# Performance work log

Hardware: AMD Instinct MI355X
Metric: run time of the kernel (lower is better)

Reference implementation:

```python
import jax, jax.numpy as jnp
import numpy as np
import math

C = 512         # embed_size
L_V = 196       # num_patches (square -> no cls token)
B_V = 64        # image batch
B_T = 32        # caption batch
N_WORD = 24     # words per caption (all cap_lens equal)
SPARSE_RATIO = 0.5
AGGR_RATIO = 0.5
NUM_KEEP = math.ceil(L_V * SPARSE_RATIO)            # 98 kept tokens
KEEPED = int(L_V * AGGR_RATIO * SPARSE_RATIO)       # 49 aggregated tokens
HIDDEN = int(C * 0.2)                               # 102 MLP hidden (dim_ratio=0.2)
LAMBDA = 4.0                                        # xattn softmax temperature
LN_EPS = 1e-5


def l2norm(x, axis=-1):
    n = jnp.linalg.norm(x, axis=axis, keepdims=True)
    return x / jnp.maximum(n, 1e-12)


def setup_inputs() -> dict:
    key = jax.random.key(0)
    ks = jax.random.split(key, 4)
    img_embs = jax.random.normal(ks[0], (B_V, L_V, C), dtype=jnp.float32)
    cap_embs = jax.random.normal(ks[1], (B_T, N_WORD, C), dtype=jnp.float32)
    cap_lens = jnp.full((B_T,), N_WORD, dtype=jnp.int64 if jax.config.read('jax_enable_x64') else jnp.int32)
    # TokenAggregation params: LayerNorm -> Linear(C,HIDDEN) -> GELU -> Linear(HIDDEN,KEEPED), scale
    ln_gamma = jnp.ones((C,), jnp.float32)
    ln_beta = jnp.zeros((C,), jnp.float32)
    W1 = jax.random.normal(ks[2], (C, HIDDEN), dtype=jnp.float32) * 0.02
    b1 = jnp.zeros((HIDDEN,), jnp.float32)
    W2 = jax.random.normal(ks[3], (HIDDEN, KEEPED), dtype=jnp.float32) * 0.02
    b2 = jnp.zeros((KEEPED,), jnp.float32)
    scale = jnp.ones((), jnp.float32)
    return dict(img_embs=img_embs, cap_embs=cap_embs, cap_lens=cap_lens,
                ln_gamma=ln_gamma, ln_beta=ln_beta, W1=W1, b1=b1, W2=W2, b2=b2, scale=scale)


def _forward(img_embs, cap_embs, ln_gamma, ln_beta, W1, b1, W2, b2, scale):
    # --- global attention scores (computed under no_grad in torch) ---
    img_norm = l2norm(img_embs)                                   # (Bv,Lv,C)
    cap_norm = l2norm(cap_embs)                                   # (Bt,W,C)
    img_glo = l2norm(jnp.mean(img_embs, axis=1, keepdims=True))   # (Bv,1,C)
    self_attn = jnp.sum(img_glo * img_norm, axis=-1)              # (Bv,Lv)
    cap_glo = l2norm(jnp.mean(cap_embs, axis=1))                  # (Bt,C)
    cross_attn = jnp.einsum('tc,vlc->tvl', cap_glo, img_norm)     # (Bt,Bv,Lv)
    score = jax.lax.stop_gradient(self_attn[None] + cross_attn)   # (Bt,Bv,Lv)

    # --- TokenSparse: sort, split keep / non-keep ---
    order = jnp.argsort(-score, axis=-1)                          # descending indices
    score_sort = jnp.take_along_axis(score, order, axis=-1)
    keep_idx = order[..., :NUM_KEEP]                              # (Bt,Bv,K)
    non_idx = order[..., NUM_KEEP:]                               # (Bt,Bv,Lv-K)
    rank = jnp.argsort(order, axis=-1)                            # inverse permutation
    score_mask = (rank < NUM_KEEP).astype(score.dtype)            # (Bt,Bv,Lv)

    bidx = jnp.arange(B_V)[None, :, None]
    select_tokens = img_embs[bidx, keep_idx]                      # (Bt,Bv,K,C) gather
    non_tokens = img_embs[bidx, non_idx]                          # (Bt,Bv,Lv-K,C)
    non_w = jax.nn.softmax(score_sort[..., NUM_KEEP:], axis=-1)   # (Bt,Bv,Lv-K)
    extra_token = jnp.sum(non_tokens * non_w[..., None], axis=-2, keepdims=True)  # (Bt,Bv,1,C)

    # --- TokenAggregation: LN -> MLP -> softmax -> bmm ---
    mu = jnp.mean(select_tokens, axis=-1, keepdims=True)
    var = jnp.var(select_tokens, axis=-1, keepdims=True)
    xn = (select_tokens - mu) * jax.lax.rsqrt(var + LN_EPS) * ln_gamma + ln_beta
    h = jax.nn.gelu(jnp.einsum('tvkc,ch->tvkh', xn, W1) + b1, approximate=False)
    w = jnp.einsum('tvkh,hp->tvkp', h, W2) + b2                   # (Bt,Bv,K,P)
    w = jnp.swapaxes(w, -1, -2) * scale                           # (Bt,Bv,P,K)
    w = jax.nn.softmax(w, axis=-1)
    aggr = jnp.einsum('tvpk,tvkc->tvpc', w, select_tokens)        # (Bt,Bv,P,C)

    keep_tokens = jnp.concatenate([aggr, extra_token], axis=2)    # (Bt,Bv,P+1,C)
    sel_norm = l2norm(keep_tokens)

    # --- mask_xattn_one_text: SCAN-style t2i attention ---
    sims = jnp.einsum('twc,tvpc->tvwp', cap_norm, sel_norm)       # (Bt,Bv,W,P+1)
    attn = jax.nn.softmax(LAMBDA * sims, axis=-1)
    ctx = l2norm(jnp.einsum('tvwp,tvpc->tvwc', attn, sel_norm))   # (Bt,Bv,W,C)
    word_sim = jnp.einsum('twc,tvwc->tvw', cap_norm, ctx)         # (Bt,Bv,W)
    sim = jnp.mean(word_sim, axis=-1)                             # (Bt,Bv)
    improve_sims = sim.T                                          # (Bv,Bt)
    return improve_sims, score_mask


def reference(img_embs, cap_embs, cap_lens, ln_gamma, ln_beta, W1, b1, W2, b2, scale):
    # cap_lens are all N_WORD (constant), so the per-caption loop is fully vectorized.
    return _forward(img_embs, cap_embs, ln_gamma, ln_beta, W1, b1, W2, b2, scale)
```

## Files before the change

### kernel.cpp

```cpp
#include <hip/hip_runtime.h>
#include <hip/hip_bf16.h>
#include <math.h>

#define CDIM 512
#define LV 196
#define BV 64
#define BT 32
#define NW 24
#define NKEEP 98
#define NNON 98
#define KEEPED 49
#define HID 102
#define LAMBDA_ 4.0f
#define LN_EPS_ 1e-5f

#define WS_CAPNORM 0
#define WS_CAPGLO  (WS_CAPNORM + BT*NW*CDIM)
#define WS_IMGGLO  (WS_CAPGLO + BT*CDIM)
#define WS_INVN    (WS_IMGGLO + BV*CDIM)
#define WS_WLOG    (WS_INVN + BV*LV)
#define WS_SCORE   (WS_WLOG + BV*LV*KEEPED)
#define WS_END     (WS_SCORE + BT*BV*LV)
#define WS_IMGT_B  ((size_t)WS_END * 4)
#define TOKPAD 224
#define WS_NEED_B  (WS_IMGT_B + (size_t)BV * CDIM * TOKPAD * 2)
#define WS_W1T_B   ((size_t)WS_SCORE * 4)
#define WS_W2T_B   (WS_W1T_B + (size_t)112 * 512 * 2)
#define WS_IPART   WS_WLOG

typedef short v8s __attribute__((ext_vector_type(8)));
typedef float v4f __attribute__((ext_vector_type(4)));
#define MFMA16(a, b, c) __builtin_amdgcn_mfma_f32_16x16x32_bf16((a), (b), (c), 0, 0, 0)

#define WA_STR 232
#define TOK_STR 40
#define SEL_STR 520
#define G_STR 66
#define XN_STR 520
#define HB_STR 136

#define SELQ_STR 136
#define CAPQ_STR 136
#define K4_SMEM   51968
#define OFF_SEL   0
#define OFF_WA    19216
#define OFF_CAPQ  19216
#define OFF_SIMS  19216
#define OFF_G     27408
#define OFF_SC    48912
#define OFF_KIDX  49696
#define OFF_NIDX  50088
#define OFF_CNT   50480
#define OFF_WK    50496
#define OFF_RED   50896
#define OFF_POOL2 51408
#define OFF_INV   51664

__device__ __forceinline__ ushort bfb(float f) {
  __hip_bfloat16 h = __float2bfloat16(f);
  union { __hip_bfloat16 h; ushort u; } cv; cv.h = h; return cv.u;
}

__global__ __launch_bounds__(512) void k0_prep(const float* __restrict__ img,
                                               const float* __restrict__ W1,
                                               const float* __restrict__ W2,
                                               float* __restrict__ ws) {
  int v = blockIdx.x, kt = blockIdx.y, c = threadIdx.x;
  if (kt == 7) {
    if (v < 56) {
      #pragma unroll
      for (int r = 0; r < 2; ++r) {
        int h = v * 2 + r;
        float val = (h < HID) ? W1[(size_t)c * HID + h] : 0.f;
        ((ushort*)((char*)ws + WS_W1T_B))[(size_t)h * 512 + c] = bfb(val);
      }
    } else {
      for (int e = c; e < 1024; e += 512) {
        int idx = (v - 56) * 1024 + e;
        int p = idx >> 7, h = idx & 127;
        float val = (p < KEEPED && h < HID) ? W2[(size_t)h * KEEPED + p] : 0.f;
        ((ushort*)((char*)ws + WS_W2T_B))[(size_t)p * 128 + h] = bfb(val);
      }
    }
    return;
  }
  float x[32];
  #pragma unroll
  for (int kk = 0; kk < 32; ++kk) {
    int tok = kt * 32 + kk;
    x[kk] = (tok < LV) ? img[((size_t)v * LV + tok) * CDIM + c] : 0.f;
  }
  {
    float s = 0.f;
    #pragma unroll
    for (int kk = 0; kk < 32; ++kk) s += x[kk];
    ws[WS_IPART + ((size_t)kt * BV + v) * CDIM + c] = s;
  }
  __hip_bfloat16* imgT = (__hip_bfloat16*)((char*)ws + WS_IMGT_B);
  uint* dst = (uint*)(imgT + ((size_t)v * CDIM + c) * TOKPAD + kt * 32);
  #pragma unroll
  for (int g = 0; g < 4; ++g) {
    uint4 u;
    u.x = (uint)bfb(x[g*8+0]) | ((uint)bfb(x[g*8+1]) << 16);
    u.y = (uint)bfb(x[g*8+2]) | ((uint)bfb(x[g*8+3]) << 16);
    u.z = (uint)bfb(x[g*8+4]) | ((uint)bfb(x[g*8+5]) << 16);
    u.w = (uint)bfb(x[g*8+6]) | ((uint)bfb(x[g*8+7]) << 16);
    *(uint4*)(dst + g * 4) = u;
  }
}

__global__ __launch_bounds__(512) void k5_prep(const float* __restrict__ W1,
                                               const float* __restrict__ W2,
                                               float* __restrict__ ws) {
  int b = blockIdx.x, tid = threadIdx.x;
  if (b < 112) {
    int h = b;
    float val = (h < HID) ? W1[(size_t)tid * HID + h] : 0.f;
    ((ushort*)((char*)ws + WS_W1T_B))[(size_t)h * 512 + tid] = bfb(val);
  } else {
    int p = b - 112;
    if (tid < 128) {
      int h = tid;
      float val = (p < KEEPED && h < HID) ? W2[(size_t)h * KEEPED + p] : 0.f;
      ((ushort*)((char*)ws + WS_W2T_B))[(size_t)p * 128 + h] = bfb(val);
    }
  }
}

template<int BIG>
__global__ __launch_bounds__(256) void k1_glo(const float* __restrict__ img,
                                              const float* __restrict__ cap,
                                              float* __restrict__ ws) {
  __shared__ float red[256];
  __shared__ float s_part[4 * CDIM];
  __shared__ float s_glo[CDIM];
  int b = blockIdx.x, tid = threadIdx.x;
  if (b < BT) {
    int t = b;
    int wv = tid >> 6, lane = tid & 63;
    int cb = lane * 8;
    float4 sA = make_float4(0.f,0.f,0.f,0.f), sB = make_float4(0.f,0.f,0.f,0.f);
    for (int w = wv; w < NW; w += 4) {
      const float* p = cap + ((size_t)t * NW + w) * CDIM + cb;
      float4 xa = *(const float4*)p;
      float4 xb = *(const float4*)(p + 4);
      float ss = xa.x*xa.x + xa.y*xa.y + xa.z*xa.z + xa.w*xa.w
               + xb.x*xb.x + xb.y*xb.y + xb.z*xb.z + xb.w*xb.w;
      #pragma unroll
      for (int off = 32; off > 0; off >>= 1) ss += __shfl_xor(ss, off, 64);
      float inv = 1.f / fmaxf(sqrtf(ss), 1e-12f);
      float* q = ws + WS_CAPNORM + ((size_t)t * NW + w) * CDIM + cb;
      *(float4*)q       = make_float4(xa.x*inv, xa.y*inv, xa.z*inv, xa.w*inv);
      *(float4*)(q + 4) = make_float4(xb.x*inv, xb.y*inv, xb.z*inv, xb.w*inv);
      sA.x += xa.x; sA.y += xa.y; sA.z += xa.z; sA.w += xa.w;
      sB.x += xb.x; sB.y += xb.y; sB.z += xb.z; sB.w += xb.w;
    }
    *(float4*)&s_part[wv * CDIM + cb]     = sA;
    *(float4*)&s_part[wv * CDIM + cb + 4] = sB;
    __syncthreads();
    if (tid < 128) {
      float4 g = make_float4(0.f, 0.f, 0.f, 0.f);
      #pragma unroll
      for (int w2 = 0; w2 < 4; ++w2) {
        float4 pv = *(const float4*)&s_part[w2 * CDIM + tid * 4];
        g.x += pv.x; g.y += pv.y; g.z += pv.z; g.w += pv.w;
      }
      g.x /= (float)NW; g.y /= (float)NW; g.z /= (float)NW; g.w /= (float)NW;
      *(float4*)&s_glo[tid * 4] = g;
      red[tid] = g.x*g.x + g.y*g.y + g.z*g.z + g.w*g.w;
    }
    __syncthreads();
    for (int off = 64; off > 0; off >>= 1) {
      if (tid < off) red[tid] += red[tid + off];
      __syncthreads();
    }
    float inv = 1.f / fmaxf(sqrtf(red[0]), 1e-12f);
    if (tid < 128) {
      float4 g = *(const float4*)&s_glo[tid * 4];
      *(float4*)(ws + WS_CAPGLO + (size_t)t * CDIM + tid * 4) =
          make_float4(g.x*inv, g.y*inv, g.z*inv, g.w*inv);
    }
  } else if (BIG) {
    int v = b - BT;
    int c0 = tid, c1 = tid + 256;
    float s0 = 0.f, s1 = 0.f;
    #pragma unroll
    for (int kt = 0; kt < 7; ++kt) {
      s0 += ws[WS_IPART + ((size_t)kt * BV + v) * CDIM + c0];
      s1 += ws[WS_IPART + ((size_t)kt * BV + v) * CDIM + c1];
    }
    float g0 = s0 / (float)LV, g1 = s1 / (float)LV;
    red[tid] = g0 * g0 + g1 * g1;
    __syncthreads();
    for (int off = 128; off > 0; off >>= 1) {
      if (tid < off) red[tid] += red[tid + off];
      __syncthreads();
    }
    float inv = 1.f / fmaxf(sqrtf(red[0]), 1e-12f);
    float* q = ws + WS_IMGGLO + (size_t)v * CDIM;
    q[c0] = g0 * inv; q[c1] = g1 * inv;
  } else {
    int v = b - BT;
    int wv = tid >> 6, lane = tid & 63;
    int cb = lane * 8;
    const float* base = img + (size_t)v * LV * CDIM;
    float4 sA = make_float4(0.f,0.f,0.f,0.f), sB = make_float4(0.f,0.f,0.f,0.f);
    int l0 = wv * 49;
    for (int l = l0; l < l0 + 49; ++l) {
      const float* p = base + (size_t)l * CDIM + cb;
      float4 xa = *(const float4*)p;
      float4 xb = *(const float4*)(p + 4);
      sA.x += xa.x; sA.y += xa.y; sA.z += xa.z; sA.w += xa.w;
      sB.x += xb.x; sB.y += xb.y; sB.z += xb.z; sB.w += xb.w;
    }
    *(float4*)&s_part[wv * CDIM + cb]     = sA;
    *(float4*)&s_part[wv * CDIM + cb + 4] = sB;
    __syncthreads();
    if (tid < 128) {
      float4 g = make_float4(0.f, 0.f, 0.f, 0.f);
      #pragma unroll
      for (int w2 = 0; w2 < 4; ++w2) {
        float4 pv = *(const float4*)&s_part[w2 * CDIM + tid * 4];
        g.x += pv.x; g.y += pv.y; g.z += pv.z; g.w += pv.w;
      }
      g.x /= (float)LV; g.y /= (float)LV; g.z /= (float)LV; g.w /= (float)LV;
      *(float4*)&s_glo[tid * 4] = g;
      red[tid] = g.x*g.x + g.y*g.y + g.z*g.z + g.w*g.w;
    }
    __syncthreads();
    for (int off = 64; off > 0; off >>= 1) {
      if (tid < off) red[tid] += red[tid + off];
      __syncthreads();
    }
    float inv = 1.f / fmaxf(sqrtf(red[0]), 1e-12f);
    if (tid < 128) {
      float4 g = *(const float4*)&s_glo[tid * 4];
      *(float4*)(ws + WS_IMGGLO + (size_t)v * CDIM + tid * 4) =
          make_float4(g.x*inv, g.y*inv, g.z*inv, g.w*inv);
    }
  }
}

__global__ __launch_bounds__(512, 4) void k2_mlp(const float* __restrict__ img,
                                                 const float* __restrict__ gamma,
                                                 const float* __restrict__ beta,
                                                 const float* __restrict__ b1,
                                                 const float* __restrict__ b2,
                                                 float* __restrict__ ws) {
  __shared__ __align__(16) __hip_bfloat16 s_xn[32 * XN_STR];
  __hip_bfloat16* s_hb = s_xn;

  int v = blockIdx.x, seg = blockIdx.y;
  int l0 = seg * 28;
  int tid = threadIdx.x, wv = tid >> 6, lane = tid & 63;
  int quad = lane >> 4, l15 = lane & 15, koff = quad * 8;
  const __hip_bfloat16* W1T = (const __hip_bfloat16*)((const char*)ws + WS_W1T_B);
  const __hip_bfloat16* W2T = (const __hip_bfloat16*)((const char*)ws + WS_W2T_B);

  int cb = lane * 8;
  float4 g4a = *(const float4*)(gamma + cb);
  float4 g4b = *(const float4*)(gamma + cb + 4);
  float4 b4a = *(const float4*)(beta + cb);
  float4 b4b = *(const float4*)(beta + cb + 4);
  for (int tok = wv; tok < 28; tok += 8) {
    const float* p = img + ((size_t)v * LV + l0 + tok) * CDIM + cb;
    float4 xa = *(const float4*)p;
    float4 xb = *(const float4*)(p + 4);
    float s  = xa.x + xa.y + xa.z + xa.w + xb.x + xb.y + xb.z + xb.w;
    float sq = xa.x*xa.x + xa.y*xa.y + xa.z*xa.z + xa.w*xa.w
             + xb.x*xb.x + xb.y*xb.y + xb.z*xb.z + xb.w*xb.w;
    #pragma unroll
    for (int off = 32; off > 0; off >>= 1) { s += __shfl_xor(s, off, 64); sq += __shfl_xor(sq, off, 64); }
    float mean = s / (float)CDIM;
    float var = sq / (float)CDIM - mean * mean;
    float rstd = 1.f / sqrtf(var + LN_EPS_);
    if (lane == 0) ws[WS_INVN + (size_t)v * LV + l0 + tok] = 1.f / fmaxf(sqrtf(sq), 1e-12f);
    float f[8];
    f[0] = (xa.x - mean) * rstd * g4a.x + b4a.x;
    f[1] = (xa.y - mean) * rstd * g4a.y + b4a.y;
    f[2] = (xa.z - mean) * rstd * g4a.z + b4a.z;
    f[3] = (xa.w - mean) * rstd * g4a.w + b4a.w;
    f[4] = (xb.x - mean) * rstd * g4b.x + b4b.x;
    f[5] = (xb.y - mean) * rstd * g4b.y + b4b.y;
    f[6] = (xb.z - mean) * rstd * g4b.z + b4b.z;
    f[7] = (xb.w - mean) * rstd * g4b.w + b4b.w;
    uint4 u;
    u.x = (uint)bfb(f[0]) | ((uint)bfb(f[1]) << 16);
    u.y = (uint)bfb(f[2]) | ((uint)bfb(f[3]) << 16);
    u.z = (uint)bfb(f[4]) | ((uint)bfb(f[5]) << 16);
    u.w = (uint)bfb(f[6]) | ((uint)bfb(f[7]) << 16);
    *(uint4*)(s_xn + (size_t)tok * XN_STR + cb) = u;
  }
  __syncthreads();

  v4f c1[2];
  int mt_[2], nt_[2];
  #pragma unroll
  for (int i = 0; i < 2; ++i) {
    int idx = wv + 8 * i; if (idx > 13) idx = 13;
    mt_[i] = idx / 7; nt_[i] = idx % 7;
    c1[i] = (v4f){0.f, 0.f, 0.f, 0.f};
  }
  for (int ks = 0; ks < 16; ++ks) {
    #pragma unroll
    for (int i = 0; i < 2; ++i) {
      v8s a  = *(const v8s*)(s_xn + (size_t)(mt_[i] * 16 + l15) * XN_STR + ks * 32 + koff);
      v8s bb = *(const v8s*)(W1T + (size_t)(nt_[i] * 16 + l15) * 512 + ks * 32 + koff);
      c1[i] = MFMA16(a, bb, c1[i]);
    }
  }
  __syncthreads();

  #pragma unroll
  for (int i = 0; i < 2; ++i) {
    int idx = wv + 8 * i;
    if (idx < 14) {
      int h = nt_[i] * 16 + l15;
      float bias = (h < HID) ? b1[h] : 0.f;
      #pragma unroll
      for (int reg = 0; reg < 4; ++reg) {
        int row = mt_[i] * 16 + quad * 4 + reg;
        float x = c1[i][reg] + bias;
        float gl = (h < HID) ? 0.5f * x * (1.f + erff(x * 0.70710678118654752f)) : 0.f;
        s_hb[(size_t)row * HB_STR + h] = __float2bfloat16(gl);
      }
    }
  }
  for (int i = tid; i < 32 * 16; i += 512)
    s_hb[(size_t)(i >> 4) * HB_STR + 112 + (i & 15)] = __float2bfloat16(0.f);
  __syncthreads();

  int m2 = wv >> 2, n2 = wv & 3;
  v4f c2 = (v4f){0.f, 0.f, 0.f, 0.f};
  for (int ks = 0; ks < 4; ++ks) {
    v8s a  = *(const v8s*)(s_hb + (size_t)(m2 * 16 + l15) * HB_STR + ks * 32 + koff);
    v8s bb = *(const v8s*)(W2T + (size_t)(n2 * 16 + l15) * 128 + ks * 32 + koff);
    c2 = MFMA16(a, bb, c2);
  }
  {
    int p = n2 * 16 + l15;
    if (p < KEEPED) {
      float bias = b2[p];
      #pragma unroll
      for (int reg = 0; reg < 4; ++reg) {
        int tok = m2 * 16 + quad * 4 + reg;
        if (tok < 28)
          ws[WS_WLOG + ((size_t)v * LV + l0 + tok) * KEEPED + p] = c2[reg] + bias;
      }
    }
  }
}

__global__ __launch_bounds__(512) void k3_score(const float* __restrict__ img,
                                                float* __restrict__ ws) {
  __shared__ __align__(16) float qt[33 * 64];
  __shared__ __align__(16) float xt[64 * 66];
  __shared__ float dself[64];
  int v = blockIdx.x;
  int t0 = blockIdx.y * 64;
  int tid = threadIdx.x;
  int tloc = tid & 63, qg = tid >> 6;
  float acc[5];
  #pragma unroll
  for (int i = 0; i < 5; ++i) acc[i] = 0.f;
  const float* capglo = ws + WS_CAPGLO;
  const float* imgglo = ws + WS_IMGGLO + (size_t)v * CDIM;

  for (int ct = 0; ct < 8; ++ct) {
    for (int i = tid; i < 33 * 64; i += 512) {
      int q = i >> 6, cc = i & 63;
      qt[i] = (q < 32) ? capglo[(size_t)q * CDIM + ct * 64 + cc] : imgglo[ct * 64 + cc];
    }
    for (int i = tid; i < 64 * 64; i += 512) {
      int tok = i >> 6, cc = i & 63;
      int l = t0 + tok;
      xt[tok * 66 + cc] = (l < LV) ? img[((size_t)v * LV + l) * CDIM + ct * 64 + cc] : 0.f;
    }
    __syncthreads();
    for (int cc2 = 0; cc2 < 32; ++cc2) {
      float2 xv = *(const float2*)&xt[tloc * 66 + cc2 * 2];
      #pragma unroll
      for (int qi = 0; qi < 5; ++qi) {
        int q = qg + 8 * qi;
        if (q < 33) {
          float2 qv = *(const float2*)&qt[q * 64 + cc2 * 2];
          acc[qi] += qv.x * xv.x;
          acc[qi] += qv.y * xv.y;
        }
      }
    }
    __syncthreads();
  }
  if (qg == 0) dself[tloc] = acc[4];
  __syncthreads();
  int l = t0 + tloc;
  if (l < LV) {
    float invn = ws[WS_INVN + (size_t)v * LV + l];
    float ds = dself[tloc];
    #pragma unroll
    for (int qi = 0; qi < 5; ++qi) {
      int q = qg + 8 * qi;
      if (q < 32) ws[WS_SCORE + ((size_t)q * BV + v) * LV + l] = (acc[qi] + ds) * invn;
    }
  }
}

template<int USE_IMGT>
__global__ __launch_bounds__(512, 2) void k4_main(const float* __restrict__ img,
                                                  const float* __restrict__ scale_p,
                                                  const float* __restrict__ ws,
                                                  float* __restrict__ out) {
  __shared__ float s_sc[LV];
  __shared__ int   s_kidx[NKEEP];
  __shared__ int   s_nidx[NNON];
  __shared__ int   s_cnt[2];
  __shared__ float s_wk[NNON];
  __shared__ float s_red[128];
  __shared__ float s_pool2[64];
  __shared__ float s_inv[64];
  __shared__ __align__(16) __hip_bfloat16 s_selh[64 * SEL_STR];
  __shared__ __align__(16) __hip_bfloat16 s_wa[64 * WA_STR];
  __shared__ __align__(16) __hip_bfloat16 s_dyn[512 * TOK_STR];

  float* s_w = (float*)s_dyn;
  __hip_bfloat16* s_tok = s_dyn;
  __hip_bfloat16* s_cap = s_dyn;
  float* s_sims = (float*)s_wa;
  float* s_G = (float*)((char*)s_wa + 8192);

  int b = blockIdx.x;
  int v = b >> 5, t = b & 31;
  int tid = threadIdx.x;
  int wv = tid >> 6, lane = tid & 63;
  int quad = lane >> 4, l15 = lane & 15;
  int koff = quad * 8;

  if (tid < 2) s_cnt[tid] = 0;
  if (tid < 64) s_pool2[tid] = 0.f;
  if (tid < LV) s_sc[tid] = ws[WS_SCORE + ((size_t)t * BV + v) * LV + tid];
  {
    uint* za = (uint*)s_wa;
    for (int i = tid; i < 64 * WA_STR / 2; i += 512) za[i] = 0u;
    uint* zs = (uint*)(s_selh + 50 * SEL_STR);
    for (int i = tid; i < 14 * SEL_STR / 2; i += 512) zs[i] = 0u;
  }
  __syncthreads();

  if (tid < LV) {
    float my = s_sc[tid];
    int cnt = 0;
    for (int j = 0; j < LV; ++j) {
      float sj = s_sc[j];
      cnt += (sj > my) || (sj == my && j < tid);
    }
    bool keep = cnt < NKEEP;
    out[BV * BT + ((size_t)t * BV + v) * LV + tid] = keep ? 1.f : 0.f;
    if (keep) { int p = atomicAdd(&s_cnt[0], 1); s_kidx[p] = tid; }
    else      { int p = atomicAdd(&s_cnt[1], 1); s_nidx[p] = tid; }
  }
  __syncthreads();

  if (tid < 128) s_red[tid] = (tid < NNON) ? s_sc[s_nidx[tid]] : -3.0e38f;
  __syncthreads();
  for (int off = 64; off > 0; off >>= 1) {
    if (tid < off) s_red[tid] = fmaxf(s_red[tid], s_red[tid + off]);
    __syncthreads();
  }
  float nm = s_red[0];
  __syncthreads();
  float e0 = 0.f;
  if (tid < NNON) e0 = expf(s_sc[s_nidx[tid]] - nm);
  if (tid < 128) s_red[tid] = (tid < NNON) ? e0 : 0.f;
  __syncthreads();
  for (int off = 64; off > 0; off >>= 1) {
    if (tid < off) s_red[tid] += s_red[tid + off];
    __syncthreads();
  }
  float nS = s_red[0];
  __syncthreads();
  if (tid < NNON) s_wk[tid] = e0 / nS;
  __syncthreads();

  float scale_val = scale_p[0];
  for (int i = tid; i < KEEPED * NKEEP; i += 512) {
    int k = i / KEEPED, p = i - k * KEEPED;
    s_w[p * NKEEP + k] = ws[WS_WLOG + ((size_t)v * LV + s_kidx[k]) * KEEPED + p] * scale_val;
  }
  __syncthreads();
  if (tid < KEEPED * 8) {
    int p = tid >> 3, g = tid & 7;
    float mm = -3e38f;
    for (int k = g; k < NKEEP; k += 8) mm = fmaxf(mm, s_w[p * NKEEP + k]);
    #pragma unroll
    for (int off = 4; off > 0; off >>= 1) mm = fmaxf(mm, __shfl_xor(mm, off, 8));
    float ss = 0.f;
    for (int k = g; k < NKEEP; k += 8) {
      float ee = expf(s_w[p * NKEEP + k] - mm);
      s_w[p * NKEEP + k] = ee;
      ss += ee;
    }
    #pragma unroll
    for (int off = 4; off > 0; off >>= 1) ss += __shfl_xor(ss, off, 8);
    float rs = 1.f / ss;
    for (int k = g; k < NKEEP; k += 8) s_w[p * NKEEP + k] *= rs;
  }
  __syncthreads();

  for (int i = tid; i < KEEPED * NKEEP; i += 512) {
    int p = i / NKEEP, r = i - p * NKEEP;
    s_wa[p * WA_STR + s_kidx[r]] = __float2bfloat16(s_w[p * NKEEP + r]);
  }
  if (tid < NNON) s_wa[49 * WA_STR + s_nidx[tid]] = __float2bfloat16(s_wk[tid]);
  __syncthreads();

  v4f acc[4][4];
  #pragma unroll
  for (int m = 0; m < 4; ++m)
    #pragma unroll
    for (int j = 0; j < 4; ++j) acc[m][j] = (v4f){0.f, 0.f, 0.f, 0.f};

  if (USE_IMGT) {
    const __hip_bfloat16* imgTv =
        (const __hip_bfloat16*)((const char*)ws + WS_IMGT_B) + (size_t)v * CDIM * TOKPAD;
    for (int ks = 0; ks < 7; ++ks) {
      v8s bfr[4];
      #pragma unroll
      for (int j = 0; j < 4; ++j)
        bfr[j] = *(const v8s*)(imgTv + (size_t)(wv * 64 + j * 16 + l15) * TOKPAD + ks * 32 + koff);
      #pragma unroll
      for (int m = 0; m < 4; ++m) {
        v8s af = *(const v8s*)(s_wa + (m * 16 + l15) * WA_STR + ks * 32 + koff);
        #pragma unroll
        for (int j = 0; j < 4; ++j) acc[m][j] = MFMA16(af, bfr[j], acc[m][j]);
      }
    }
  } else {
    for (int ks = 0; ks < 7; ++ks) {
      #pragma unroll
      for (int it = 0; it < 8; ++it) {
        int k0 = ks * 32 + it * 4;
        if (k0 < LV) {
          const float* gp = img + ((size_t)v * LV + k0) * CDIM + tid;
          float x0 = gp[0], x1 = gp[CDIM], x2 = gp[2 * CDIM], x3 = gp[3 * CDIM];
          union { __hip_bfloat16 h[4]; uint2 u; } pk;
          pk.h[0] = __float2bfloat16(x0); pk.h[1] = __float2bfloat16(x1);
          pk.h[2] = __float2bfloat16(x2); pk.h[3] = __float2bfloat16(x3);
          *(uint2*)(s_tok + tid * TOK_STR + it * 4) = pk.u;
        }
      }
      __syncthreads();
      v8s bfr[4];
      #pragma unroll
      for (int j = 0; j < 4; ++j)
        bfr[j] = *(const v8s*)(s_tok + (wv * 64 + j * 16 + l15) * TOK_STR + koff);
      #pragma unroll
      for (int m = 0; m < 4; ++m) {
        v8s af = *(const v8s*)(s_wa + (m * 16 + l15) * WA_STR + ks * 32 + koff);
        #pragma unroll
        for (int j = 0; j < 4; ++j) acc[m][j] = MFMA16(af, bfr[j], acc[m][j]);
      }
      __syncthreads();
    }
  }

  if (!USE_IMGT) __syncthreads();
  for (int i = tid; i < NW * 128; i += 512) {
    int w = i >> 7, cq = i & 127;
    const float4 xv = *(const float4*)(ws + WS_CAPNORM + ((size_t)t * NW + w) * CDIM + cq * 4);
    union { __hip_bfloat16 h[4]; uint2 u; } pk;
    pk.h[0] = __float2bfloat16(xv.x); pk.h[1] = __float2bfloat16(xv.y);
    pk.h[2] = __float2bfloat16(xv.z); pk.h[3] = __float2bfloat16(xv.w);
    *(uint2*)(s_cap + w * SEL_STR + cq * 4) = pk.u;
  }
  {
    uint* zc = (uint*)(s_cap + 24 * SEL_STR);
    for (int i = tid; i < 8 * SEL_STR / 2; i += 512) zc[i] = 0u;
  }
  #pragma unroll
  for (int m = 0; m < 4; ++m) {
    #pragma unroll
    for (int reg = 0; reg < 4; ++reg) {
      float ss = acc[m][0][reg] * acc[m][0][reg] + acc[m][1][reg] * acc[m][1][reg]
               + acc[m][2][reg] * acc[m][2][reg] + acc[m][3][reg] * acc[m][3][reg];
      #pragma unroll
      for (int off = 8; off > 0; off >>= 1) ss += __shfl_xor(ss, off, 64);
      if (l15 == 0) atomicAdd(&s_pool2[m * 16 + quad * 4 + reg], ss);
    }
  }
  __syncthreads();
  if (tid < 64) s_inv[tid] = 1.f / fmaxf(sqrtf(s_pool2[tid]), 1e-12f);
  __syncthreads();
  #pragma unroll
  for (int m = 0; m < 4; ++m) {
    #pragma unroll
    for (int reg = 0; reg < 4; ++reg) {
      int p = m * 16 + quad * 4 + reg;
      if (p < 50) {
        float iv = s_inv[p];
        #pragma unroll
        for (int j = 0; j < 4; ++j)
          s_selh[p * SEL_STR + wv * 64 + j * 16 + l15] = __float2bfloat16(acc[m][j][reg] * iv);
      }
    }
  }
  __syncthreads();

  {
    int mt = wv >> 2, nt = wv & 3;
    v4f sa = (v4f){0.f, 0.f, 0.f, 0.f};
    for (int ks = 0; ks < 16; ++ks) {
      v8s a = *(const v8s*)(s_cap + (mt * 16 + l15) * SEL_STR + ks * 32 + koff);
      v8s bb = *(const v8s*)(s_selh + (nt * 16 + l15) * SEL_STR + ks * 32 + koff);
      sa = MFMA16(a, bb, sa);
    }
    #pragma unroll
    for (int reg = 0; reg < 4; ++reg)
      s_sims[(mt * 16 + quad * 4 + reg) * 64 + nt * 16 + l15] = sa[reg];
  }
  __syncthreads();

  if (tid < NW * 8) {
    int w = tid >> 3, g = tid & 7;
    float* row = s_sims + w * 64;
    float mm = -3e38f;
    for (int p = g; p < 50; p += 8) mm = fmaxf(mm, row[p]);
    #pragma unroll
    for (int off = 4; off > 0; off >>= 1) mm = fmaxf(mm, __shfl_xor(mm, off, 8));
    float num = 0.f;
    for (int p = g; p < 64; p += 8) {
      if (p < 50) {
        float s = row[p];
        float ee = expf(LAMBDA_ * (s - mm));
        num += ee * s;
        row[p] = ee;
      } else row[p] = 0.f;
    }
    #pragma unroll
    for (int off = 4; off > 0; off >>= 1) num += __shfl_xor(num, off, 8);
    if (g == 0) s_red[w] = num;
  }
  __syncthreads();

  #pragma unroll
  for (int i2 = 0; i2 < 2; ++i2) {
    int idx = wv * 2 + i2;
    int gm = idx >> 2, gn = idx & 3;
    v4f ga = (v4f){0.f, 0.f, 0.f, 0.f};
    for (int ks = 0; ks < 16; ++ks) {
      v8s a = *(const v8s*)(s_selh + (gm * 16 + l15) * SEL_STR + ks * 32 + koff);
      v8s bb = *(const v8s*)(s_selh + (gn * 16 + l15) * SEL_STR + ks * 32 + koff);
      ga = MFMA16(a, bb, ga);
    }
    #pragma unroll
    for (int reg = 0; reg < 4; ++reg)
      s_G[(gm * 16 + quad * 4 + reg) * G_STR + gn * 16 + l15] = ga[reg];
  }
  __syncthreads();

  float wacc = 0.f;
  for (int w = wv; w < NW; w += 8) {
    const float* ev = s_sims + w * 64;
    float tl = 0.f;
    for (int q = 0; q < 50; ++q) tl += s_G[q * G_STR + lane] * ev[q];
    float ql = ev[lane] * tl;
    #pragma unroll
    for (int off = 32; off > 0; off >>= 1) ql += __shfl_xor(ql, off, 64);
    if (lane == 0) wacc += s_red[w] / fmaxf(sqrtf(ql), 1e-20f);
  }
  if (lane == 0) s_red[64 + wv] = wacc;
  __syncthreads();
  if (tid == 0) {
    float s = 0.f;
    #pragma unroll
    for (int i = 0; i < 8; ++i) s += s_red[64 + i];
    out[(size_t)v * BT + t] = s / (float)NW;
  }
}

__global__ __launch_bounds__(512, 4) void k4_big(const float* __restrict__ img,
                                                 const float* __restrict__ scale_p,
                                                 const float* __restrict__ ws,
                                                 float* __restrict__ out) {
  __shared__ __align__(16) char smem[K4_SMEM];
  __hip_bfloat16* s_sel = (__hip_bfloat16*)(smem + OFF_SEL);
  float*          s_w   = (float*)(smem + OFF_SEL);
  __hip_bfloat16* s_wa  = (__hip_bfloat16*)(smem + OFF_WA);
  __hip_bfloat16* s_capq= (__hip_bfloat16*)(smem + OFF_CAPQ);
  float*          s_sims= (float*)(smem + OFF_SIMS);
  float*          s_G   = (float*)(smem + OFF_G);
  float* s_sc    = (float*)(smem + OFF_SC);
  int*   s_kidx  = (int*)(smem + OFF_KIDX);
  int*   s_nidx  = (int*)(smem + OFF_NIDX);
  int*   s_cnt   = (int*)(smem + OFF_CNT);
  float* s_wk    = (float*)(smem + OFF_WK);
  float* s_red   = (float*)(smem + OFF_RED);
  float* s_pool2 = (float*)(smem + OFF_POOL2);
  float* s_inv   = (float*)(smem + OFF_INV);

  int b0 = blockIdx.x;
  int b = ((b0 & 7) << 8) | (b0 >> 3);
  int v = b >> 5, t = b & 31;
  int tid = threadIdx.x;
  int wv = tid >> 6, lane = tid & 63;
  int quad = lane >> 4, l15 = lane & 15;
  int koff = quad * 8;

  if (tid < 2) s_cnt[tid] = 0;
  if (tid < 64) s_pool2[tid] = 0.f;
  if (tid < LV) s_sc[tid] = ws[WS_SCORE + ((size_t)t * BV + v) * LV + tid];
  {
    uint* za = (uint*)s_wa;
    for (int i = tid; i < 64 * WA_STR / 2; i += 512) za[i] = 0u;
  }
  __syncthreads();

  if (tid < LV) {
    float my = s_sc[tid];
    int cnt = 0;
    for (int j = 0; j < LV; ++j) {
      float sj = s_sc[j];
      cnt += (sj > my) || (sj == my && j < tid);
    }
    bool keep = cnt < NKEEP;
    out[BV * BT + ((size_t)t * BV + v) * LV + tid] = keep ? 1.f : 0.f;
    if (keep) { int p = atomicAdd(&s_cnt[0], 1); s_kidx[p] = tid; }
    else      { int p = atomicAdd(&s_cnt[1], 1); s_nidx[p] = tid; }
  }
  __syncthreads();

  if (tid < 128) {
    float vmax = (tid < NNON) ? s_sc[s_nidx[tid]] : -3.0e38f;
    #pragma unroll
    for (int off = 32; off > 0; off >>= 1) vmax = fmaxf(vmax, __shfl_xor(vmax, off, 64));
    if ((tid & 63) == 0) s_red[tid >> 6] = vmax;
  }
  __syncthreads();
  float nm = fmaxf(s_red[0], s_red[1]);
  float e0 = 0.f;
  if (tid < 128) {
    float vs = 0.f;
    if (tid < NNON) { e0 = expf(s_sc[s_nidx[tid]] - nm); vs = e0; }
    #pragma unroll
    for (int off = 32; off > 0; off >>= 1) vs += __shfl_xor(vs, off, 64);
    if ((tid & 63) == 0) s_red[2 + (tid >> 6)] = vs;
  }
  __syncthreads();
  float nS = s_red[2] + s_red[3];
  if (tid < NNON) s_wk[tid] = e0 / nS;
  __syncthreads();

  float scale_val = scale_p[0];
  for (int i = tid; i < KEEPED * NKEEP; i += 512) {
    int k = i / KEEPED, p = i - k * KEEPED;
    s_w[p * NKEEP + k] = ws[WS_WLOG + ((size_t)v * LV + s_kidx[k]) * KEEPED + p] * scale_val;
  }
  __syncthreads();
  if (tid < KEEPED * 8) {
    int p = tid >> 3, g = tid & 7;
    float mm = -3e38f;
    for (int k = g; k < NKEEP; k += 8) mm = fmaxf(mm, s_w[p * NKEEP + k]);
    #pragma unroll
    for (int off = 4; off > 0; off >>= 1) mm = fmaxf(mm, __shfl_xor(mm, off, 8));
    float ss = 0.f;
    for (int k = g; k < NKEEP; k += 8) {
      float ee = expf(s_w[p * NKEEP + k] - mm);
      s_w[p * NKEEP + k] = ee;
      ss += ee;
    }
    #pragma unroll
    for (int off = 4; off > 0; off >>= 1) ss += __shfl_xor(ss, off, 8);
    float rs = 1.f / ss;
    for (int k = g; k < NKEEP; k += 8) s_w[p * NKEEP + k] *= rs;
  }
  __syncthreads();

  for (int i = tid; i < KEEPED * NKEEP; i += 512) {
    int p = i / NKEEP, r = i - p * NKEEP;
    s_wa[p * WA_STR + s_kidx[r]] = __float2bfloat16(s_w[p * NKEEP + r]);
  }
  if (tid < NNON) s_wa[49 * WA_STR + s_nidx[tid]] = __float2bfloat16(s_wk[tid]);
  __syncthreads();

  {
    uint* zq = (uint*)(s_sel + 50 * SELQ_STR);
    for (int i = tid; i < 14 * SELQ_STR / 2; i += 512) zq[i] = 0u;
  }

  v4f acc[4][4];
  #pragma unroll
  for (int m = 0; m < 4; ++m)
    #pragma unroll
    for (int j = 0; j < 4; ++j) acc[m][j] = (v4f){0.f, 0.f, 0.f, 0.f};

  {
    const __hip_bfloat16* imgTv =
        (const __hip_bfloat16*)((const char*)ws + WS_IMGT_B) + (size_t)v * CDIM * TOKPAD;
    for (int ks = 0; ks < 7; ++ks) {
      v8s bfr[4];
      #pragma unroll
      for (int j = 0; j < 4; ++j)
        bfr[j] = *(const v8s*)(imgTv + (size_t)(wv * 64 + j * 16 + l15) * TOKPAD + ks * 32 + koff);
      #pragma unroll
      for (int m = 0; m < 4; ++m) {
        v8s af = *(const v8s*)(s_wa + (m * 16 + l15) * WA_STR + ks * 32 + koff);
        #pragma unroll
        for (int j = 0; j < 4; ++j) acc[m][j] = MFMA16(af, bfr[j], acc[m][j]);
      }
    }
  }

  #pragma unroll
  for (int m = 0; m < 4; ++m) {
    #pragma unroll
    for (int reg = 0; reg < 4; ++reg) {
      float ss = acc[m][0][reg] * acc[m][0][reg] + acc[m][1][reg] * acc[m][1][reg]
               + acc[m][2][reg] * acc[m][2][reg] + acc[m][3][reg] * acc[m][3][reg];
      #pragma unroll
      for (int off = 8; off > 0; off >>= 1) ss += __shfl_xor(ss, off, 64);
      if (l15 == 0) atomicAdd(&s_pool2[m * 16 + quad * 4 + reg], ss);
    }
  }
  __syncthreads();
  if (tid < 64) s_inv[tid] = 1.f / fmaxf(sqrtf(s_pool2[tid]), 1e-12f);
  __syncthreads();

  uint pk[4][4][2];
  #pragma unroll
  for (int m = 0; m < 4; ++m) {
    #pragma unroll
    for (int rp = 0; rp < 2; ++rp) {
      int p0 = m * 16 + quad * 4 + rp * 2;
      float iv0 = s_inv[p0], iv1 = s_inv[p0 + 1];
      #pragma unroll
      for (int j = 0; j < 4; ++j)
        pk[m][j][rp] = (uint)bfb(acc[m][j][2 * rp] * iv0)
                     | ((uint)bfb(acc[m][j][2 * rp + 1] * iv1) << 16);
    }
  }

  v4f sa = (v4f){0.f, 0.f, 0.f, 0.f};
  v4f ga[2];
  ga[0] = (v4f){0.f, 0.f, 0.f, 0.f};
  ga[1] = (v4f){0.f, 0.f, 0.f, 0.f};
  ushort* selw = (ushort*)s_sel;
  int mt = wv >> 2, nt = wv & 3;
  for (int q = 0; q < 4; ++q) {
    if ((wv >> 1) == q) {
      int base = (wv & 1) * 64;
      #pragma unroll
      for (int m = 0; m < 4; ++m) {
        #pragma unroll
        for (int reg = 0; reg < 4; ++reg) {
          int p = m * 16 + quad * 4 + reg;
          if (p < 50) {
            #pragma unroll
            for (int j = 0; j < 4; ++j) {
              uint u = pk[m][j][reg >> 1];
              ushort val = (reg & 1) ? (ushort)(u >> 16) : (ushort)(u & 0xffffu);
              selw[p * SELQ_STR + base + j * 16 + l15] = val;
            }
          }
        }
      }
    } else {
      int rank = wv - (wv > 2 * q + 1 ? 2 : 0);
      int lt = rank * 64 + lane;
      for (int i = lt; i < NW * 32; i += 384) {
        int w = i >> 5, c4 = i & 31;
        float4 xv = *(const float4*)(ws + WS_CAPNORM + ((size_t)t * NW + w) * CDIM
                                     + q * 128 + c4 * 4);
        union { __hip_bfloat16 hh[4]; uint2 u; } pc;
        pc.hh[0] = __float2bfloat16(xv.x); pc.hh[1] = __float2bfloat16(xv.y);
        pc.hh[2] = __float2bfloat16(xv.z); pc.hh[3] = __float2bfloat16(xv.w);
        *(uint2*)(s_capq + w * CAPQ_STR + c4 * 4) = pc.u;
      }
    }
    __syncthreads();
    #pragma unroll
    for (int ks = 0; ks < 4; ++ks) {
      v8s a  = *(const v8s*)(s_capq + (mt * 16 + l15) * CAPQ_STR + ks * 32 + koff);
      v8s bb = *(const v8s*)(s_sel + (nt * 16 + l15) * SELQ_STR + ks * 32 + koff);
      sa = MFMA16(a, bb, sa);
    }
    #pragma unroll
    for (int i2 = 0; i2 < 2; ++i2) {
      int idx = wv * 2 + i2;
      int gm = idx >> 2, gn = idx & 3;
      #pragma unroll
      for (int ks = 0; ks < 4; ++ks) {
        v8s a  = *(const v8s*)(s_sel + (gm * 16 + l15) * SELQ_STR + ks * 32 + koff);
        v8s bb = *(const v8s*)(s_sel + (gn * 16 + l15) * SELQ_STR + ks * 32 + koff);
        ga[i2] = MFMA16(a, bb, ga[i2]);
      }
    }
    __syncthreads();
  }

  #pragma unroll
  for (int reg = 0; reg < 4; ++reg)
    s_sims[(mt * 16 + quad * 4 + reg) * 64 + nt * 16 + l15] = sa[reg];
  #pragma unroll
  for (int i2 = 0; i2 < 2; ++i2) {
    int idx = wv * 2 + i2;
    int gm = idx >> 2, gn = idx & 3;
    #pragma unroll
    for (int reg = 0; reg < 4; ++reg)
      s_G[(gm * 16 + quad * 4 + reg) * G_STR + gn * 16 + l15] = ga[i2][reg];
  }
  __syncthreads();

  if (tid < NW * 8) {
    int w = tid >> 3, g = tid & 7;
    float* row = s_sims + w * 64;
    float mm = -3e38f;
    for (int p = g; p < 50; p += 8) mm = fmaxf(mm, row[p]);
    #pragma unroll
    for (int off = 4; off > 0; off >>= 1) mm = fmaxf(mm, __shfl_xor(mm, off, 8));
    float num = 0.f;
    for (int p = g; p < 64; p += 8) {
      if (p < 50) {
        float s = row[p];
        float ee = expf(LAMBDA_ * (s - mm));
        num += ee * s;
        row[p] = ee;
      } else row[p] = 0.f;
    }
    #pragma unroll
    for (int off = 4; off > 0; off >>= 1) num += __shfl_xor(num, off, 8);
    if (g == 0) s_red[w] = num;
  }
  __syncthreads();

  float wacc = 0.f;
  for (int w = wv; w < NW; w += 8) {
    const float* ev = s_sims + w * 64;
    float tl = 0.f;
    for (int q = 0; q < 50; ++q) tl += s_G[q * G_STR + lane] * ev[q];
    float ql = ev[lane] * tl;
    #pragma unroll
    for (int off = 32; off > 0; off >>= 1) ql += __shfl_xor(ql, off, 64);
    if (lane == 0) wacc += s_red[w] / fmaxf(sqrtf(ql), 1e-20f);
  }
  if (lane == 0) s_red[64 + wv] = wacc;
  __syncthreads();
  if (tid == 0) {
    float s = 0.f;
    #pragma unroll
    for (int i = 0; i < 8; ++i) s += s_red[64 + i];
    out[(size_t)v * BT + t] = s / (float)NW;
  }
}

extern "C" void kernel_launch(void* const* d_in, const int* in_sizes, int n_in,
                              void* d_out, int out_size, void* d_ws, size_t ws_size,
                              hipStream_t stream) {
  const float* img   = (const float*)d_in[0];
  const float* cap   = (const float*)d_in[1];
  const float* gamma = (const float*)d_in[3];
  const float* beta  = (const float*)d_in[4];
  const float* W1    = (const float*)d_in[5];
  const float* b1    = (const float*)d_in[6];
  const float* W2    = (const float*)d_in[7];
  const float* b2    = (const float*)d_in[8];
  const float* scale = (const float*)d_in[9];
  float* ws  = (float*)d_ws;
  float* out = (float*)d_out;

  const bool big = (ws_size >= WS_NEED_B);

  if (big) {
    k0_prep<<<dim3(BV, 8), dim3(512), 0, stream>>>(img, W1, W2, ws);
    k1_glo<1><<<dim3(BT + BV), dim3(256), 0, stream>>>(img, cap, ws);
  } else {
    k5_prep<<<dim3(176), dim3(512), 0, stream>>>(W1, W2, ws);
    k1_glo<0><<<dim3(BT + BV), dim3(256), 0, stream>>>(img, cap, ws);
  }
  k2_mlp <<<dim3(BV, 7), dim3(512), 0, stream>>>(img, gamma, beta, b1, b2, ws);
  k3_score<<<dim3(BV, 4), dim3(512), 0, stream>>>(img, ws);
  if (big) k4_big<<<dim3(BV * BT), dim3(512), 0, stream>>>(img, scale, ws, out);
  else     k4_main<0><<<dim3(BV * BT), dim3(512), 0, stream>>>(img, scale, ws, out);
}
```

Before: 303.2 us.

## Fold caption/image global pooling into prep and MLP kernels, widen score blocks

```diff
diff --git a/kernel.cpp b/kernel.cpp
--- a/kernel.cpp
+++ b/kernel.cpp
@@ -26,7 +26,7 @@
 #define WS_NEED_B  (WS_IMGT_B + (size_t)BV * CDIM * TOKPAD * 2)
 #define WS_W1T_B   ((size_t)WS_SCORE * 4)
 #define WS_W2T_B   (WS_W1T_B + (size_t)112 * 512 * 2)
-#define WS_IPART   WS_WLOG
+#define WS_IPART   (WS_SCORE + 40960)
 
 typedef short v8s __attribute__((ext_vector_type(8)));
 typedef float v4f __attribute__((ext_vector_type(4)));
@@ -62,10 +62,62 @@
 }
 
 __global__ __launch_bounds__(512) void k0_prep(const float* __restrict__ img,
+                                               const float* __restrict__ cap,
                                                const float* __restrict__ W1,
                                                const float* __restrict__ W2,
                                                float* __restrict__ ws) {
+  __shared__ float s_part[8 * CDIM];
+  __shared__ float s_glo[CDIM];
+  __shared__ float red[128];
   int v = blockIdx.x, kt = blockIdx.y, c = threadIdx.x;
+  if (kt == 8) {
+    if (v >= BT) return;
+    int t = v;
+    int wv = c >> 6, lane = c & 63;
+    int cb = lane * 8;
+    float4 sA = make_float4(0.f,0.f,0.f,0.f), sB = make_float4(0.f,0.f,0.f,0.f);
+    for (int w = wv; w < NW; w += 8) {
+      const float* p = cap + ((size_t)t * NW + w) * CDIM + cb;
+      float4 xa = *(const float4*)p;
+      float4 xb = *(const float4*)(p + 4);
+      float ss = xa.x*xa.x + xa.y*xa.y + xa.z*xa.z + xa.w*xa.w
+               + xb.x*xb.x + xb.y*xb.y + xb.z*xb.z + xb.w*xb.w;
+      #pragma unroll
+      for (int off = 32; off > 0; off >>= 1) ss += __shfl_xor(ss, off, 64);
+      float inv = 1.f / fmaxf(sqrtf(ss), 1e-12f);
+      float* q = ws + WS_CAPNORM + ((size_t)t * NW + w) * CDIM + cb;
+      *(float4*)q       = make_float4(xa.x*inv, xa.y*inv, xa.z*inv, xa.w*inv);
+      *(float4*)(q + 4) = make_float4(xb.x*inv, xb.y*inv, xb.z*inv, xb.w*inv);
+      sA.x += xa.x; sA.y += xa.y; sA.z += xa.z; sA.w += xa.w;
+      sB.x += xb.x; sB.y += xb.y; sB.z += xb.z; sB.w += xb.w;
+    }
+    *(float4*)&s_part[wv * CDIM + cb]     = sA;
+    *(float4*)&s_part[wv * CDIM + cb + 4] = sB;
+    __syncthreads();
+    if (c < 128) {
+      float4 g = make_float4(0.f, 0.f, 0.f, 0.f);
+      #pragma unroll
+      for (int w2 = 0; w2 < 8; ++w2) {
+        float4 pv = *(const float4*)&s_part[w2 * CDIM + c * 4];
+        g.x += pv.x; g.y += pv.y; g.z += pv.z; g.w += pv.w;
+      }
+      g.x /= (float)NW; g.y /= (float)NW; g.z /= (float)NW; g.w /= (float)NW;
+      *(float4*)&s_glo[c * 4] = g;
+      red[c] = g.x*g.x + g.y*g.y + g.z*g.z + g.w*g.w;
+    }
+    __syncthreads();
+    for (int off = 64; off > 0; off >>= 1) {
+      if (c < off) red[c] += red[c + off];
+      __syncthreads();
+    }
+    float inv = 1.f / fmaxf(sqrtf(red[0]), 1e-12f);
+    if (c < 128) {
+      float4 g = *(const float4*)&s_glo[c * 4];
+      *(float4*)(ws + WS_CAPGLO + (size_t)t * CDIM + c * 4) =
+          make_float4(g.x*inv, g.y*inv, g.z*inv, g.w*inv);
+    }
+    return;
+  }
   if (kt == 7) {
     if (v < 56) {
       #pragma unroll
@@ -127,7 +179,6 @@
   }
 }
 
-template<int BIG>
 __global__ __launch_bounds__(256) void k1_glo(const float* __restrict__ img,
                                               const float* __restrict__ cap,
                                               float* __restrict__ ws) {
@@ -180,25 +231,6 @@
       *(float4*)(ws + WS_CAPGLO + (size_t)t * CDIM + tid * 4) =
           make_float4(g.x*inv, g.y*inv, g.z*inv, g.w*inv);
     }
-  } else if (BIG) {
-    int v = b - BT;
-    int c0 = tid, c1 = tid + 256;
-    float s0 = 0.f, s1 = 0.f;
-    #pragma unroll
-    for (int kt = 0; kt < 7; ++kt) {
-      s0 += ws[WS_IPART + ((size_t)kt * BV + v) * CDIM + c0];
-      s1 += ws[WS_IPART + ((size_t)kt * BV + v) * CDIM + c1];
-    }
-    float g0 = s0 / (float)LV, g1 = s1 / (float)LV;
-    red[tid] = g0 * g0 + g1 * g1;
-    __syncthreads();
-    for (int off = 128; off > 0; off >>= 1) {
-      if (tid < off) red[tid] += red[tid + off];
-      __syncthreads();
-    }
-    float inv = 1.f / fmaxf(sqrtf(red[0]), 1e-12f);
-    float* q = ws + WS_IMGGLO + (size_t)v * CDIM;
-    q[c0] = g0 * inv; q[c1] = g1 * inv;
   } else {
     int v = b - BT;
     int wv = tid >> 6, lane = tid & 63;
@@ -251,8 +283,32 @@
   __hip_bfloat16* s_hb = s_xn;
 
   int v = blockIdx.x, seg = blockIdx.y;
+  int tid = threadIdx.x, wv = tid >> 6, lane = tid & 63;
+
+  if (seg == 7) {
+    float* sc = (float*)s_xn;
+    float s0 = 0.f;
+    #pragma unroll
+    for (int kt = 0; kt < 7; ++kt)
+      s0 += ws[WS_IPART + ((size_t)kt * BV + v) * CDIM + tid];
+    float g = s0 / (float)LV;
+    float ss = g * g;
+    #pragma unroll
+    for (int off = 32; off > 0; off >>= 1) ss += __shfl_xor(ss, off, 64);
+    if (lane == 0) sc[wv] = ss;
+    __syncthreads();
+    if (tid == 0) {
+      float tot = 0.f;
+      #pragma unroll
+      for (int i = 0; i < 8; ++i) tot += sc[i];
+      sc[8] = 1.f / fmaxf(sqrtf(tot), 1e-12f);
+    }
+    __syncthreads();
+    ws[WS_IMGGLO + (size_t)v * CDIM + tid] = g * sc[8];
+    return;
+  }
+
   int l0 = seg * 28;
-  int tid = threadIdx.x, wv = tid >> 6, lane = tid & 63;
   int quad = lane >> 4, l15 = lane & 15, koff = quad * 8;
   const __hip_bfloat16* W1T = (const __hip_bfloat16*)((const char*)ws + WS_W1T_B);
   const __hip_bfloat16* W2T = (const __hip_bfloat16*)((const char*)ws + WS_W2T_B);
@@ -351,8 +407,8 @@
   }
 }
 
-__global__ __launch_bounds__(512) void k3_score(const float* __restrict__ img,
-                                                float* __restrict__ ws) {
+__global__ __launch_bounds__(1024) void k3_score(const float* __restrict__ img,
+                                                 float* __restrict__ ws) {
   __shared__ __align__(16) float qt[33 * 64];
   __shared__ __align__(16) float xt[64 * 66];
   __shared__ float dself[64];
@@ -360,18 +416,18 @@
   int t0 = blockIdx.y * 64;
   int tid = threadIdx.x;
   int tloc = tid & 63, qg = tid >> 6;
-  float acc[5];
-  #pragma unroll
-  for (int i = 0; i < 5; ++i) acc[i] = 0.f;
+  float acc[3];
+  #pragma unroll
+  for (int i = 0; i < 3; ++i) acc[i] = 0.f;
   const float* capglo = ws + WS_CAPGLO;
   const float* imgglo = ws + WS_IMGGLO + (size_t)v * CDIM;
 
   for (int ct = 0; ct < 8; ++ct) {
-    for (int i = tid; i < 33 * 64; i += 512) {
+    for (int i = tid; i < 33 * 64; i += 1024) {
       int q = i >> 6, cc = i & 63;
       qt[i] = (q < 32) ? capglo[(size_t)q * CDIM + ct * 64 + cc] : imgglo[ct * 64 + cc];
     }
-    for (int i = tid; i < 64 * 64; i += 512) {
+    for (int i = tid; i < 64 * 64; i += 1024) {
       int tok = i >> 6, cc = i & 63;
       int l = t0 + tok;
       xt[tok * 66 + cc] = (l < LV) ? img[((size_t)v * LV + l) * CDIM + ct * 64 + cc] : 0.f;
@@ -380,8 +436,8 @@
     for (int cc2 = 0; cc2 < 32; ++cc2) {
       float2 xv = *(const float2*)&xt[tloc * 66 + cc2 * 2];
       #pragma unroll
-      for (int qi = 0; qi < 5; ++qi) {
-        int q = qg + 8 * qi;
+      for (int qi = 0; qi < 3; ++qi) {
+        int q = qg + 16 * qi;
         if (q < 33) {
           float2 qv = *(const float2*)&qt[q * 64 + cc2 * 2];
           acc[qi] += qv.x * xv.x;
@@ -391,15 +447,15 @@
     }
     __syncthreads();
   }
-  if (qg == 0) dself[tloc] = acc[4];
+  if (qg == 0) dself[tloc] = acc[2];
   __syncthreads();
   int l = t0 + tloc;
   if (l < LV) {
     float invn = ws[WS_INVN + (size_t)v * LV + l];
     float ds = dself[tloc];
     #pragma unroll
-    for (int qi = 0; qi < 5; ++qi) {
-      int q = qg + 8 * qi;
+    for (int qi = 0; qi < 3; ++qi) {
+      int q = qg + 16 * qi;
       if (q < 32) ws[WS_SCORE + ((size_t)q * BV + v) * LV + l] = (acc[qi] + ds) * invn;
     }
   }
@@ -969,14 +1025,14 @@
   const bool big = (ws_size >= WS_NEED_B);
 
   if (big) {
-    k0_prep<<<dim3(BV, 8), dim3(512), 0, stream>>>(img, W1, W2, ws);
-    k1_glo<1><<<dim3(BT + BV), dim3(256), 0, stream>>>(img, cap, ws);
+    k0_prep<<<dim3(BV, 9), dim3(512), 0, stream>>>(img, cap, W1, W2, ws);
+    k2_mlp <<<dim3(BV, 8), dim3(512), 0, stream>>>(img, gamma, beta, b1, b2, ws);
   } else {
     k5_prep<<<dim3(176), dim3(512), 0, stream>>>(W1, W2, ws);
-    k1_glo<0><<<dim3(BT + BV), dim3(256), 0, stream>>>(img, cap, ws);
-  }
-  k2_mlp <<<dim3(BV, 7), dim3(512), 0, stream>>>(img, gamma, beta, b1, b2, ws);
-  k3_score<<<dim3(BV, 4), dim3(512), 0, stream>>>(img, ws);
+    k1_glo <<<dim3(BT + BV), dim3(256), 0, stream>>>(img, cap, ws);
+    k2_mlp <<<dim3(BV, 7), dim3(512), 0, stream>>>(img, gamma, beta, b1, b2, ws);
+  }
+  k3_score<<<dim3(BV, 4), dim3(1024), 0, stream>>>(img, ws);
   if (big) k4_big<<<dim3(BV * BT), dim3(512), 0, stream>>>(img, scale, ws, out);
   else     k4_main<0><<<dim3(BV * BT), dim3(512), 0, stream>>>(img, scale, ws, out);
 }
```

Result: faster. 286.6 us (-5.5%).
